# Kernel optimization log

Hardware: AMD Instinct MI355X
Metric: run time of the kernel (lower is better)

## Reference

```python
import jax, jax.numpy as jnp
import numpy as np

NUM_INPUTS = 8
N_MF = 4
NUM_RULES = N_MF ** NUM_INPUTS  # 65536
BATCH = 1024


def setup_inputs() -> dict:
    key = jax.random.key(0)
    k1, k2, k3, k4 = jax.random.split(key, 4)
    x = jax.random.normal(k1, (BATCH, NUM_INPUTS), dtype=jnp.float32)
    mu = jax.random.normal(k2, (NUM_INPUTS, N_MF), dtype=jnp.float32)
    sigma = jnp.ones((NUM_INPUTS, N_MF), dtype=jnp.float32)
    consequent_weights = jax.random.normal(k3, (NUM_RULES, NUM_INPUTS), dtype=jnp.float32)
    consequent_bias = jax.random.normal(k4, (NUM_RULES,), dtype=jnp.float32)
    return {"x": x, "mu": mu, "sigma": sigma,
            "consequent_weights": consequent_weights,
            "consequent_bias": consequent_bias}


def reference(x, mu, sigma, consequent_weights, consequent_bias):
    # Gaussian memberships: (B, num_inputs, n_mf)
    inv_two_var = 1.0 / (2.0 * jnp.square(jnp.abs(sigma) + 1e-5))
    membership = jnp.exp(-jnp.square(x[:, :, None] - mu) * inv_two_var)

    # Combinatorial rule strengths: iterated outer product over inputs.
    # itertools.product ordering => input 0 is the most-significant index,
    # which matches left-to-right outer-product flattening.
    B = x.shape[0]
    w = membership[:, 0, :]  # (B, n_mf)
    for i in range(1, NUM_INPUTS):
        w = (w[:, :, None] * membership[:, i, None, :]).reshape(B, -1)
    # w: (B, num_rules)

    w_norm = w / (jnp.sum(w, axis=1, keepdims=True) + 1e-6)

    # First-order consequents: (B, num_rules)
    rule_outputs = jnp.einsum('bi,ri->br', x, consequent_weights) + consequent_bias

    return jnp.sum(w_norm * rule_outputs, axis=1, keepdims=True)  # (B, 1)
```

## Files before the change

### kernel.cpp

```cpp
#include <hip/hip_runtime.h>

typedef _Float16 half2v __attribute__((ext_vector_type(2)));
typedef _Float16 half8v __attribute__((ext_vector_type(8)));
typedef float floatx4 __attribute__((ext_vector_type(4)));

#define NBATCH 1024
#define NKSPLIT 128
#define KPW 16
#define NMTILE 16
#define MSPAD 36
#define NPART 32

__device__ __forceinline__ float sel4(float a0, float a1, float a2, float a3, int d) {
  float r = (d == 1) ? a1 : a0;
  r = (d == 2) ? a2 : r;
  r = (d == 3) ? a3 : r;
  return r;
}

__device__ __forceinline__ half2v cvt2h(float a, float b) {
  return __builtin_bit_cast(half2v, __builtin_amdgcn_cvt_pkrtz(a, b));
}

__global__ __launch_bounds__(256, 2) void anfis_main(
    const float* __restrict__ x, const float* __restrict__ mu,
    const float* __restrict__ sigma, const float* __restrict__ cw,
    const float* __restrict__ cb, float* __restrict__ part) {
  const int bid = blockIdx.x;
  const int mtile = bid >> 5;
  const int kq = bid & 31;
  const int t = threadIdx.x;
  const int w = t >> 6;
  const int l = t & 63;
  const int g = l >> 4, col = l & 15;
  const int u = g & 1, h = g >> 1;
  const int ksplit = kq * 4 + w;
  const int d0 = (ksplit >> 5) & 3, d1 = (ksplit >> 3) & 3, d2 = (ksplit >> 1) & 3;
  const int d3h = ksplit & 1;
  const int b0 = mtile * 64;
  const int r0 = ksplit * (KPW * 32) + g * 8;

  const bool isw = (col < 8);
  const float* gp = isw ? (cw + (size_t)r0 * 8 + col) : (cb + r0);
  const int es = isw ? 8 : 1;
  const int ks = isw ? 256 : 32;

  float fv[4][8];
#pragma unroll
  for (int kk = 0; kk < 4; ++kk)
#pragma unroll
    for (int e = 0; e < 8; ++e)
      fv[kk][e] = gp[kk * ks + e * es];

  __shared__ float msL[64][MSPAD];
  __shared__ float bsum[4][64];
  {
    const int bt = t >> 2;
    const int j0 = (t & 3) * 8;
#pragma unroll
    for (int j = 0; j < 8; ++j) {
      const int jj = j0 + j;
      const int i = jj >> 2;
      float s_ = fabsf(sigma[jj]) + 1e-5f;
      float rs = __builtin_amdgcn_rcpf(s_);
      float nv = -0.5f * rs * rs;
      float d = x[(b0 + bt) * 8 + i] - mu[jj];
      msL[bt][jj] = __expf(d * d * nv);
    }
  }
  __syncthreads();

  half2v tab[4][4];
  float pA[4][2], pB[4][2];
  floatx4 m4v[4];
#pragma unroll
  for (int rb = 0; rb < 4; ++rb) {
    const float* row = msL[rb * 16 + col];
    floatx4 m0 = *(const floatx4*)(row + 0);
    floatx4 m1 = *(const floatx4*)(row + 4);
    floatx4 m2 = *(const floatx4*)(row + 8);
    floatx4 m3 = *(const floatx4*)(row + 12);
    floatx4 m4 = *(const floatx4*)(row + 16);
    floatx4 m5 = *(const floatx4*)(row + 20);
    floatx4 m6 = *(const floatx4*)(row + 24);
    floatx4 m7 = *(const floatx4*)(row + 28);
    float pre = sel4(m0[0], m0[1], m0[2], m0[3], d0) *
                sel4(m1[0], m1[1], m1[2], m1[3], d1) *
                sel4(m2[0], m2[1], m2[2], m2[3], d2);
    float m3a = d3h ? m3[2] : m3[0];
    float m3b = d3h ? m3[3] : m3[1];
    float m5A = h ? m5[1] : m5[0];
    float m5B = h ? m5[3] : m5[2];
    float m60 = u ? m6[2] : m6[0];
    float m61 = u ? m6[3] : m6[1];
    tab[rb][0] = cvt2h(m60 * m7[0], m60 * m7[1]);
    tab[rb][1] = cvt2h(m60 * m7[2], m60 * m7[3]);
    tab[rb][2] = cvt2h(m61 * m7[0], m61 * m7[1]);
    tab[rb][3] = cvt2h(m61 * m7[2], m61 * m7[3]);
    float t3a = pre * m3a, t3b = pre * m3b;
    pA[rb][0] = t3a * m5A; pA[rb][1] = t3a * m5B;
    pB[rb][0] = t3b * m5A; pB[rb][1] = t3b * m5B;
    m4v[rb] = m4;
  }

  floatx4 acc[4];
#pragma unroll
  for (int rb = 0; rb < 4; ++rb) acc[rb] = (floatx4){0.f, 0.f, 0.f, 0.f};

#pragma unroll
  for (int kk = 0; kk < KPW; ++kk) {
    const int j3 = kk >> 3, j4 = (kk >> 1) & 3, j01 = kk & 1;
    half2v b01 = cvt2h(fv[kk & 3][0], fv[kk & 3][1]);
    half2v b23 = cvt2h(fv[kk & 3][2], fv[kk & 3][3]);
    half2v b45 = cvt2h(fv[kk & 3][4], fv[kk & 3][5]);
    half2v b67 = cvt2h(fv[kk & 3][6], fv[kk & 3][7]);
    half8v b8 = {b01.x, b01.y, b23.x, b23.y, b45.x, b45.y, b67.x, b67.y};
    if (kk + 4 < KPW) {
#pragma unroll
      for (int e = 0; e < 8; ++e)
        fv[kk & 3][e] = gp[(kk + 4) * ks + e * es];
    }
#pragma unroll
    for (int rb = 0; rb < 4; ++rb) {
      float p5 = (j3 ? pB[rb][j01] : pA[rb][j01]) * m4v[rb][j4];
      _Float16 ph = (_Float16)p5;
      half2v ppv = {ph, ph};
      half2v a0 = ppv * tab[rb][0], a1 = ppv * tab[rb][1],
             a2 = ppv * tab[rb][2], a3 = ppv * tab[rb][3];
      half8v a8 = {a0.x, a0.y, a1.x, a1.y, a2.x, a2.y, a3.x, a3.y};
      acc[rb] = __builtin_amdgcn_mfma_f32_16x16x32_f16(a8, b8, acc[rb], 0, 0, 0);
    }
  }

#pragma unroll
  for (int rb = 0; rb < 4; ++rb) {
#pragma unroll
    for (int i = 0; i < 4; ++i) {
      int bb = b0 + rb * 16 + g * 4 + i;
      float xc = 0.0f;
      if (col < 8) xc = x[bb * 8 + col];
      else if (col == 8) xc = 1.0f;
      float v = acc[rb][i] * xc;
      v += __shfl_xor(v, 1);
      v += __shfl_xor(v, 2);
      v += __shfl_xor(v, 4);
      v += __shfl_xor(v, 8);
      if (col == 0) bsum[w][rb * 16 + g * 4 + i] = v;
    }
  }
  __syncthreads();

  if (t < 64) {
    float tot = bsum[0][t] + bsum[1][t] + bsum[2][t] + bsum[3][t];
    part[kq * NBATCH + b0 + t] = tot;
  }
}

__global__ __launch_bounds__(64) void anfis_final(
    const float* __restrict__ part, const float* __restrict__ x,
    const float* __restrict__ mu, const float* __restrict__ sigma,
    float* __restrict__ out) {
  const int b = blockIdx.x * 64 + threadIdx.x;

  float s = 0.0f;
#pragma unroll
  for (int j = 0; j < NPART; ++j)
    s += part[j * NBATCH + b];

  const float4* xv = (const float4*)(x + b * 8);
  float4 xa = xv[0], xb = xv[1];
  float xs8[8] = {xa.x, xa.y, xa.z, xa.w, xb.x, xb.y, xb.z, xb.w};
  float den = 1.0f;
#pragma unroll
  for (int i = 0; i < 8; ++i) {
    float rowsum = 0.0f;
#pragma unroll
    for (int q = 0; q < 4; ++q) {
      float s_ = fabsf(sigma[i * 4 + q]) + 1e-5f;
      float rs = __builtin_amdgcn_rcpf(s_);
      float nvq = -0.5f * rs * rs;
      float d = xs8[i] - mu[i * 4 + q];
      rowsum += __expf(d * d * nvq);
    }
    den *= rowsum;
  }
  out[b] = s / (den + 1e-6f);
}

extern "C" void kernel_launch(void* const* d_in, const int* in_sizes, int n_in,
                              void* d_out, int out_size, void* d_ws, size_t ws_size,
                              hipStream_t stream) {
  const float* x     = (const float*)d_in[0];
  const float* mu    = (const float*)d_in[1];
  const float* sigma = (const float*)d_in[2];
  const float* cw    = (const float*)d_in[3];
  const float* cb    = (const float*)d_in[4];
  float* part = (float*)d_ws;
  float* out = (float*)d_out;

  anfis_main<<<NMTILE * 32, 256, 0, stream>>>(x, mu, sigma, cw, cb, part);
  anfis_final<<<NBATCH / 64, 64, 0, stream>>>(part, x, mu, sigma, out);
}
```

Measured before the change: 16.66 us.

## Fuse final normalization into main kernel using per-tile completion flags

Drops the separate reduction kernel. Each block publishes its partial sum with an agent-scope store and then sets a release flag. The last k-slice block of each batch tile spins on the 32 flags, sums the partials, and divides by the normalizer. The normalizer is now built from the membership values already in shared memory instead of recomputing exponentials. This removes a second kernel launch and its dependency gap, but it relies on all blocks being co-resident, on the flag workspace starting at zero, and on resetting the flags for the next call.

```diff
diff --git a/kernel.cpp b/kernel.cpp
--- a/kernel.cpp
+++ b/kernel.cpp
@@ -5,11 +5,9 @@
 typedef float floatx4 __attribute__((ext_vector_type(4)));
 
 #define NBATCH 1024
-#define NKSPLIT 128
 #define KPW 16
 #define NMTILE 16
 #define MSPAD 36
-#define NPART 32
 
 __device__ __forceinline__ float sel4(float a0, float a1, float a2, float a3, int d) {
   float r = (d == 1) ? a1 : a0;
@@ -22,10 +20,11 @@
   return __builtin_bit_cast(half2v, __builtin_amdgcn_cvt_pkrtz(a, b));
 }
 
-__global__ __launch_bounds__(256, 2) void anfis_main(
+__global__ __launch_bounds__(256, 2) void anfis_fused(
     const float* __restrict__ x, const float* __restrict__ mu,
     const float* __restrict__ sigma, const float* __restrict__ cw,
-    const float* __restrict__ cb, float* __restrict__ part) {
+    const float* __restrict__ cb, float* __restrict__ part,
+    int* __restrict__ flags, float* __restrict__ out) {
   const int bid = blockIdx.x;
   const int mtile = bid >> 5;
   const int kq = bid & 31;
@@ -152,39 +151,41 @@
 
   if (t < 64) {
     float tot = bsum[0][t] + bsum[1][t] + bsum[2][t] + bsum[3][t];
-    part[kq * NBATCH + b0 + t] = tot;
-  }
-}
-
-__global__ __launch_bounds__(64) void anfis_final(
-    const float* __restrict__ part, const float* __restrict__ x,
-    const float* __restrict__ mu, const float* __restrict__ sigma,
-    float* __restrict__ out) {
-  const int b = blockIdx.x * 64 + threadIdx.x;
-
-  float s = 0.0f;
-#pragma unroll
-  for (int j = 0; j < NPART; ++j)
-    s += part[j * NBATCH + b];
-
-  const float4* xv = (const float4*)(x + b * 8);
-  float4 xa = xv[0], xb = xv[1];
-  float xs8[8] = {xa.x, xa.y, xa.z, xa.w, xb.x, xb.y, xb.z, xb.w};
-  float den = 1.0f;
-#pragma unroll
-  for (int i = 0; i < 8; ++i) {
-    float rowsum = 0.0f;
-#pragma unroll
-    for (int q = 0; q < 4; ++q) {
-      float s_ = fabsf(sigma[i * 4 + q]) + 1e-5f;
-      float rs = __builtin_amdgcn_rcpf(s_);
-      float nvq = -0.5f * rs * rs;
-      float d = xs8[i] - mu[i * 4 + q];
-      rowsum += __expf(d * d * nvq);
-    }
-    den *= rowsum;
-  }
-  out[b] = s / (den + 1e-6f);
+    __hip_atomic_store(&part[kq * NBATCH + b0 + t], tot,
+                       __ATOMIC_RELAXED, __HIP_MEMORY_SCOPE_AGENT);
+  }
+  __syncthreads();
+  if (t == 0)
+    __hip_atomic_store(&flags[mtile * 32 + kq], 1,
+                       __ATOMIC_RELEASE, __HIP_MEMORY_SCOPE_AGENT);
+
+  if (kq == 31) {
+    if (t < 32) {
+      while (__hip_atomic_load(&flags[mtile * 32 + t],
+                               __ATOMIC_ACQUIRE, __HIP_MEMORY_SCOPE_AGENT) != 1)
+        __builtin_amdgcn_s_sleep(2);
+    }
+    __syncthreads();
+    if (t < 64) {
+      float s = 0.0f;
+#pragma unroll
+      for (int j = 0; j < 32; ++j)
+        s += __hip_atomic_load(&part[j * NBATCH + b0 + t],
+                               __ATOMIC_RELAXED, __HIP_MEMORY_SCOPE_AGENT);
+      const float* row = msL[t];
+      float den = 1.0f;
+#pragma unroll
+      for (int i = 0; i < 8; ++i) {
+        floatx4 m = *(const floatx4*)(row + i * 4);
+        den *= (m[0] + m[1] + m[2] + m[3]);
+      }
+      out[b0 + t] = s / (den + 1e-6f);
+    }
+    __syncthreads();
+    if (t < 32)
+      __hip_atomic_store(&flags[mtile * 32 + t], 0,
+                         __ATOMIC_RELAXED, __HIP_MEMORY_SCOPE_AGENT);
+  }
 }
 
 extern "C" void kernel_launch(void* const* d_in, const int* in_sizes, int n_in,
@@ -196,8 +197,8 @@
   const float* cw    = (const float*)d_in[3];
   const float* cb    = (const float*)d_in[4];
   float* part = (float*)d_ws;
-  float* out = (float*)d_out;
-
-  anfis_main<<<NMTILE * 32, 256, 0, stream>>>(x, mu, sigma, cw, cb, part);
-  anfis_final<<<NBATCH / 64, 64, 0, stream>>>(part, x, mu, sigma, out);
-}
+  int* flags  = (int*)((char*)d_ws + 32 * NBATCH * 4);
+  float* out  = (float*)d_out;
+
+  anfis_fused<<<NMTILE * 32, 256, 0, stream>>>(x, mu, sigma, cw, cb, part, flags, out);
+}
```

New measurement: 20.67 us. 24.0% more time.
